# Kernel optimization log

Measured on AMD Instinct MI355X. Metric: run time of the kernel, lower is better.

The kernel has to match this reference:

```python
import jax, jax.numpy as jnp
import numpy as np
import itertools

DIMS = (128, 128, 128)
CHANNELS = 8
BATCH = 2_097_152


def setup_inputs() -> dict:
    key = jax.random.key(0)
    k1, k2 = jax.random.split(key)
    unList = jax.random.uniform(k1, (BATCH, len(DIMS)), dtype=jnp.float32)
    table = jax.random.uniform(k2, DIMS + (CHANNELS,), dtype=jnp.float32)  # initScale=1, initMode='R'
    return {"unList": unList, "table": table}


def reference(unList, table):
    # N-D multilinear (bilinear/trilinear) interpolated table lookup.
    dims = table.shape[:-1]
    n = len(dims)
    c = table.shape[-1]
    dims_f = jnp.asarray(dims, jnp.float32)
    # map normalized coords [0,1] onto grid [0, dim-1]
    scaled = jnp.clip(unList, 0.0, 1.0) * (dims_f - 1.0)          # [B, n]
    i0 = jnp.clip(jnp.floor(scaled), 0.0, dims_f - 2.0).astype(jnp.int32)  # lower corner
    frac = scaled - i0.astype(jnp.float32)                        # [B, n] in [0,1]
    # flatten grid for single-axis gathers
    strides = jnp.asarray([int(np.prod(dims[k + 1:])) for k in range(n)], jnp.int32)
    table_flat = table.reshape(-1, c)                             # [prod(dims), C]
    out = jnp.zeros((unList.shape[0], c), table.dtype)
    # loop over the 2^n corners (8 for 3D) -- small static loop
    for corner in itertools.product((0, 1), repeat=n):
        bits = jnp.asarray(corner, jnp.int32)                     # [n]
        flat_idx = ((i0 + bits) * strides).sum(-1)                # [B]
        w = jnp.prod(jnp.where(jnp.asarray(corner, bool), frac, 1.0 - frac), axis=-1)  # [B]
        out = out + w[:, None] * table_flat[flat_idx]             # gather + weighted sum
    return out
```

## Files before the change

### kernel.cpp

```cpp
#include <hip/hip_runtime.h>


#define DIM 128
#define CH 8
#define NBIN 4064
#define TBYTES 67108864u
#define CHUNK 8192
#define PPT 32
#define CUR_OFF 16384
#define BASE_OFF 32768
#define REC_OFF 65536

__device__ __forceinline__ int key_of(float ux, float uy) {
    float sx = fminf(fmaxf(ux, 0.0f), 1.0f) * 127.0f;
    float sy = fminf(fmaxf(uy, 0.0f), 1.0f) * 127.0f;
    int x0 = (int)fminf(floorf(sx), 126.0f);
    int y0 = (int)fminf(floorf(sy), 126.0f);
    return x0 * 32 + (y0 >> 2);
}

__global__ __launch_bounds__(256) void k_hist(const float* __restrict__ un,
                                              unsigned* __restrict__ hist, int batch) {
    __shared__ unsigned lh[NBIN];
    for (int i = threadIdx.x; i < NBIN; i += 256) lh[i] = 0;
    __syncthreads();
    int stride = gridDim.x * blockDim.x;
    for (int i = blockIdx.x * blockDim.x + threadIdx.x; i < batch; i += stride)
        atomicAdd(&lh[key_of(un[3 * i], un[3 * i + 1])], 1u);
    __syncthreads();
    for (int i = threadIdx.x; i < NBIN; i += 256)
        if (lh[i]) atomicAdd(&hist[i], lh[i]);
}

__global__ __launch_bounds__(1024) void k_scan(const unsigned* __restrict__ hist,
                                               unsigned* __restrict__ cursor,
                                               unsigned* __restrict__ base) {
    __shared__ unsigned s[1024];
    int t = threadIdx.x;
    int b0 = t * 4;
    unsigned loc[4], sum = 0;
#pragma unroll
    for (int j = 0; j < 4; ++j) {
        int k = b0 + j;
        unsigned h = (k < NBIN) ? hist[k] : 0u;
        loc[j] = sum;
        sum += h;
    }
    s[t] = sum;
    __syncthreads();
    for (int off = 1; off < 1024; off <<= 1) {
        unsigned v = (t >= off) ? s[t - off] : 0u;
        __syncthreads();
        s[t] += v;
        __syncthreads();
    }
    unsigned excl = s[t] - sum;
#pragma unroll
    for (int j = 0; j < 4; ++j) {
        int k = b0 + j;
        if (k < NBIN) { base[k] = excl + loc[j]; cursor[k] = excl + loc[j]; }
    }
    if (t == 1023) base[NBIN] = s[1023];
}

__global__ __launch_bounds__(256) void k_scatter(const float* __restrict__ un,
                                                 unsigned* __restrict__ cursor,
                                                 float4* __restrict__ rec, int batch) {
    __shared__ unsigned lh[NBIN];
    __shared__ unsigned lbase[NBIN];
    int t = threadIdx.x;
    for (int i = t; i < NBIN; i += 256) lh[i] = 0;
    __syncthreads();
    int start = blockIdx.x * CHUNK;
    unsigned kr[PPT];
#pragma unroll
    for (int j = 0; j < PPT; ++j) {
        int i = start + j * 256 + t;
        if (i < batch) {
            int k = key_of(un[3 * i], un[3 * i + 1]);
            unsigned r = atomicAdd(&lh[k], 1u);
            kr[j] = (unsigned)k | (r << 12);
        } else kr[j] = 0u;
    }
    __syncthreads();
    for (int i = t; i < NBIN; i += 256)
        lbase[i] = lh[i] ? atomicAdd(&cursor[i], lh[i]) : 0u;
    __syncthreads();
#pragma unroll
    for (int j = 0; j < PPT; ++j) {
        int i = start + j * 256 + t;
        if (i < batch) {
            unsigned k = kr[j] & 4095u, r = kr[j] >> 12;
            float ux = un[3 * i], uy = un[3 * i + 1], uz = un[3 * i + 2];
            rec[lbase[k] + r] = make_float4(ux, uy, uz, __uint_as_float((unsigned)i));
        }
    }
}

__global__ __launch_bounds__(256) void k_main(const float4* __restrict__ rec,
                                              const float* __restrict__ table,
                                              const unsigned* __restrict__ base,
                                              float* __restrict__ out) {
    __shared__ float4 lds4[2560];
    char* ldsb = (char*)lds4;
    const char* tb = (const char*)table;

    int g = blockIdx.x;
    int gx = g >> 5, gy2 = g & 31;
    int ybase = gy2 * 4;
    unsigned s = base[g], e = base[g + 1];

    unsigned offA = (unsigned)(gx * 128 + ybase) * 4096u;
    unsigned offB = offA + 524288u;

    for (int i = threadIdx.x; i < 1280; i += 256) {
        unsigned go = offA + (unsigned)i * 16u;
        if (go > TBYTES - 16u) go = TBYTES - 16u;
        lds4[i] = *(const float4*)(tb + go);
    }
    for (int i = threadIdx.x; i < 1280; i += 256) {
        unsigned go = offB + (unsigned)i * 16u;
        if (go > TBYTES - 16u) go = TBYTES - 16u;
        lds4[1280 + i] = *(const float4*)(tb + go);
    }
    __syncthreads();

    int t = (int)threadIdx.x;
    int lane = t & 63, wave = t >> 6;
    int p = lane >> 2, q = lane & 3;
    const float dmax = 127.0f, imax = 126.0f;
    const unsigned qoff = (unsigned)(q << 4);

    for (unsigned i0 = s + (unsigned)(wave * 16); i0 < e; i0 += 64u) {
        unsigned i = i0 + (unsigned)p;
        if (i < e) {
            float4 r = rec[i];
            unsigned orig = __float_as_uint(r.w);

            float sx = fminf(fmaxf(r.x, 0.0f), 1.0f) * dmax;
            float sy = fminf(fmaxf(r.y, 0.0f), 1.0f) * dmax;
            float sz = fminf(fmaxf(r.z, 0.0f), 1.0f) * dmax;
            float fx0 = fminf(floorf(sx), imax);
            float fy0 = fminf(floorf(sy), imax);
            float fz0 = fminf(floorf(sz), imax);
            int y0 = (int)fy0, z0 = (int)fz0;
            float fx = sx - fx0, fy = sy - fy0, fz = sz - fz0;

            float wzq = (q & 2) ? fz : (1.0f - fz);
            float gxw = 1.0f - fx, gyw = 1.0f - fy;
            float w0 = gxw * gyw * wzq;
            float w1 = gxw * fy  * wzq;
            float w2 = fx  * gyw * wzq;
            float w3 = fx  * fy  * wzq;

            int dy = y0 - ybase;
            unsigned a = (unsigned)(dy * 4096 + z0 * 32) + qoff;

            float4 v0 = *(const float4*)(ldsb + a);
            float4 v1 = *(const float4*)(ldsb + a + 4096u);
            float4 v2 = *(const float4*)(ldsb + a + 20480u);
            float4 v3 = *(const float4*)(ldsb + a + 24576u);

            float4 acc;
            acc.x = w0 * v0.x + w1 * v1.x + w2 * v2.x + w3 * v3.x;
            acc.y = w0 * v0.y + w1 * v1.y + w2 * v2.y + w3 * v3.y;
            acc.z = w0 * v0.z + w1 * v1.z + w2 * v2.z + w3 * v3.z;
            acc.w = w0 * v0.w + w1 * v1.w + w2 * v2.w + w3 * v3.w;

            acc.x += __shfl_xor(acc.x, 2);
            acc.y += __shfl_xor(acc.y, 2);
            acc.z += __shfl_xor(acc.z, 2);
            acc.w += __shfl_xor(acc.w, 2);

            if (q < 2)
                *reinterpret_cast<float4*>(out + (size_t)orig * CH + (q << 2)) = acc;
        }
    }
}

__global__ __launch_bounds__(256) void k_naive(const float* __restrict__ un,
                                               const float* __restrict__ table,
                                               float* __restrict__ out, int batch) {
    int b = blockIdx.x * blockDim.x + threadIdx.x;
    if (b >= batch) return;
    float ux = un[3 * b], uy = un[3 * b + 1], uz = un[3 * b + 2];
    const float dmax = 127.0f, imax = 126.0f;
    float sx = fminf(fmaxf(ux, 0.0f), 1.0f) * dmax;
    float sy = fminf(fmaxf(uy, 0.0f), 1.0f) * dmax;
    float sz = fminf(fmaxf(uz, 0.0f), 1.0f) * dmax;
    float fx0 = fminf(floorf(sx), imax);
    float fy0 = fminf(floorf(sy), imax);
    float fz0 = fminf(floorf(sz), imax);
    int x0 = (int)fx0, y0 = (int)fy0, z0 = (int)fz0;
    float fx = sx - fx0, fy = sy - fy0, fz = sz - fz0;
    float wx[2] = {1.0f - fx, fx};
    float wy[2] = {1.0f - fy, fy};
    float wz0 = 1.0f - fz, wz1 = fz;
    float acc[CH];
#pragma unroll
    for (int c = 0; c < CH; ++c) acc[c] = 0.0f;
#pragma unroll
    for (int bx = 0; bx < 2; ++bx)
#pragma unroll
        for (int by = 0; by < 2; ++by) {
            const float* pp = table + ((size_t)((x0 + bx) * DIM + (y0 + by)) * DIM + z0) * CH;
            float wxy = wx[bx] * wy[by];
            float w0 = wxy * wz0, w1 = wxy * wz1;
            float4 a0 = *reinterpret_cast<const float4*>(pp + 0);
            float4 a1 = *reinterpret_cast<const float4*>(pp + 4);
            float4 b0 = *reinterpret_cast<const float4*>(pp + 8);
            float4 b1 = *reinterpret_cast<const float4*>(pp + 12);
            acc[0] += w0 * a0.x + w1 * b0.x;  acc[1] += w0 * a0.y + w1 * b0.y;
            acc[2] += w0 * a0.z + w1 * b0.z;  acc[3] += w0 * a0.w + w1 * b0.w;
            acc[4] += w0 * a1.x + w1 * b1.x;  acc[5] += w0 * a1.y + w1 * b1.y;
            acc[6] += w0 * a1.z + w1 * b1.z;  acc[7] += w0 * a1.w + w1 * b1.w;
        }
    float4* o = reinterpret_cast<float4*>(out + (size_t)b * CH);
    o[0] = make_float4(acc[0], acc[1], acc[2], acc[3]);
    o[1] = make_float4(acc[4], acc[5], acc[6], acc[7]);
}

extern "C" void kernel_launch(void* const* d_in, const int* in_sizes, int n_in,
                              void* d_out, int out_size, void* d_ws, size_t ws_size,
                              hipStream_t stream) {
    const float* un    = (const float*)d_in[0];
    const float* table = (const float*)d_in[1];
    float* out         = (float*)d_out;
    int batch = in_sizes[0] / 3;

    size_t need = (size_t)REC_OFF + (size_t)batch * 16;
    if (ws_size < need) {
        int grid = (batch + 255) / 256;
        k_naive<<<grid, 256, 0, stream>>>(un, table, out, batch);
        return;
    }

    unsigned* hist   = (unsigned*)d_ws;
    unsigned* cursor = (unsigned*)((char*)d_ws + CUR_OFF);
    unsigned* base   = (unsigned*)((char*)d_ws + BASE_OFF);
    float4*   rec    = (float4*)((char*)d_ws + REC_OFF);

    hipMemsetAsync(d_ws, 0, CUR_OFF, stream);
    k_hist<<<512, 256, 0, stream>>>(un, hist, batch);
    k_scan<<<1, 1024, 0, stream>>>(hist, cursor, base);
    int nscat = (batch + CHUNK - 1) / CHUNK;
    k_scatter<<<nscat, 256, 0, stream>>>(un, cursor, rec, batch);
    k_main<<<NBIN, 256, 0, stream>>>(rec, table, base, out);
}
```

Baseline: 129.3 us.

## Swizzle LDS tile layout and software-pipeline record loads in main kernel

The table slab is now stored in LDS under an XOR swizzle of the address bits, meant to cut bank conflicts on the per-point corner reads. The two staging loops are merged into one, and blocks with no records exit right after staging. The record loop is unrolled four ways with the next four records prefetched while the current ones are processed, so global load latency overlaps with compute. The cost is more registers and possibly lower occupancy, and the prefetch clamps to the last valid index, adding redundant reads near the end of each range.

```diff
diff --git a/kernel.cpp b/kernel.cpp
--- a/kernel.cpp
+++ b/kernel.cpp
@@ -114,68 +114,82 @@
     unsigned offB = offA + 524288u;
 
     for (int i = threadIdx.x; i < 1280; i += 256) {
-        unsigned go = offA + (unsigned)i * 16u;
+        unsigned wa = (unsigned)i * 16u;
+        unsigned sa = wa ^ ((wa >> 2) & 0x60u);
+        unsigned go = offA + wa;
         if (go > TBYTES - 16u) go = TBYTES - 16u;
-        lds4[i] = *(const float4*)(tb + go);
-    }
-    for (int i = threadIdx.x; i < 1280; i += 256) {
-        unsigned go = offB + (unsigned)i * 16u;
+        *(float4*)(ldsb + sa) = *(const float4*)(tb + go);
+        go = offB + wa;
         if (go > TBYTES - 16u) go = TBYTES - 16u;
-        lds4[1280 + i] = *(const float4*)(tb + go);
-    }
-    __syncthreads();
+        *(float4*)(ldsb + 20480u + sa) = *(const float4*)(tb + go);
+    }
+    __syncthreads();
+    if (e <= s) return;
 
     int t = (int)threadIdx.x;
     int lane = t & 63, wave = t >> 6;
     int p = lane >> 2, q = lane & 3;
     const float dmax = 127.0f, imax = 126.0f;
     const unsigned qoff = (unsigned)(q << 4);
-
-    for (unsigned i0 = s + (unsigned)(wave * 16); i0 < e; i0 += 64u) {
-        unsigned i = i0 + (unsigned)p;
-        if (i < e) {
-            float4 r = rec[i];
-            unsigned orig = __float_as_uint(r.w);
-
-            float sx = fminf(fmaxf(r.x, 0.0f), 1.0f) * dmax;
-            float sy = fminf(fmaxf(r.y, 0.0f), 1.0f) * dmax;
-            float sz = fminf(fmaxf(r.z, 0.0f), 1.0f) * dmax;
-            float fx0 = fminf(floorf(sx), imax);
-            float fy0 = fminf(floorf(sy), imax);
-            float fz0 = fminf(floorf(sz), imax);
-            int y0 = (int)fy0, z0 = (int)fz0;
-            float fx = sx - fx0, fy = sy - fy0, fz = sz - fz0;
-
-            float wzq = (q & 2) ? fz : (1.0f - fz);
-            float gxw = 1.0f - fx, gyw = 1.0f - fy;
-            float w0 = gxw * gyw * wzq;
-            float w1 = gxw * fy  * wzq;
-            float w2 = fx  * gyw * wzq;
-            float w3 = fx  * fy  * wzq;
-
-            int dy = y0 - ybase;
-            unsigned a = (unsigned)(dy * 4096 + z0 * 32) + qoff;
-
-            float4 v0 = *(const float4*)(ldsb + a);
-            float4 v1 = *(const float4*)(ldsb + a + 4096u);
-            float4 v2 = *(const float4*)(ldsb + a + 20480u);
-            float4 v3 = *(const float4*)(ldsb + a + 24576u);
-
-            float4 acc;
-            acc.x = w0 * v0.x + w1 * v1.x + w2 * v2.x + w3 * v3.x;
-            acc.y = w0 * v0.y + w1 * v1.y + w2 * v2.y + w3 * v3.y;
-            acc.z = w0 * v0.z + w1 * v1.z + w2 * v2.z + w3 * v3.z;
-            acc.w = w0 * v0.w + w1 * v1.w + w2 * v2.w + w3 * v3.w;
-
-            acc.x += __shfl_xor(acc.x, 2);
-            acc.y += __shfl_xor(acc.y, 2);
-            acc.z += __shfl_xor(acc.z, 2);
-            acc.w += __shfl_xor(acc.w, 2);
-
-            if (q < 2)
-                *reinterpret_cast<float4*>(out + (size_t)orig * CH + (q << 2)) = acc;
-        }
-    }
+    const unsigned last = e - 1u;
+
+    unsigned myi = s + (unsigned)(wave * 16 + p);
+    unsigned cnt = e - s;
+
+#define PROC(rr, idx) { \
+        if ((idx) < e) { \
+            unsigned orig = __float_as_uint(rr.w); \
+            float sx = fminf(fmaxf(rr.x, 0.0f), 1.0f) * dmax; \
+            float sy = fminf(fmaxf(rr.y, 0.0f), 1.0f) * dmax; \
+            float sz = fminf(fmaxf(rr.z, 0.0f), 1.0f) * dmax; \
+            float fx0 = fminf(floorf(sx), imax); \
+            float fy0 = fminf(floorf(sy), imax); \
+            float fz0 = fminf(floorf(sz), imax); \
+            int y0 = (int)fy0, z0 = (int)fz0; \
+            float fx = sx - fx0, fy = sy - fy0, fz = sz - fz0; \
+            float wzq = (q & 2) ? fz : (1.0f - fz); \
+            float gxw = 1.0f - fx, gyw = 1.0f - fy; \
+            float w0 = gxw * gyw * wzq; \
+            float w1 = gxw * fy  * wzq; \
+            float w2 = fx  * gyw * wzq; \
+            float w3 = fx  * fy  * wzq; \
+            int dy = y0 - ybase; \
+            unsigned a = (unsigned)(dy * 4096 + z0 * 32) + qoff; \
+            unsigned sa = a ^ ((a >> 2) & 0x60u); \
+            float4 v0 = *(const float4*)(ldsb + sa); \
+            float4 v1 = *(const float4*)(ldsb + sa + 4096u); \
+            float4 v2 = *(const float4*)(ldsb + sa + 20480u); \
+            float4 v3 = *(const float4*)(ldsb + sa + 24576u); \
+            float4 acc; \
+            acc.x = w0 * v0.x + w1 * v1.x + w2 * v2.x + w3 * v3.x; \
+            acc.y = w0 * v0.y + w1 * v1.y + w2 * v2.y + w3 * v3.y; \
+            acc.z = w0 * v0.z + w1 * v1.z + w2 * v2.z + w3 * v3.z; \
+            acc.w = w0 * v0.w + w1 * v1.w + w2 * v2.w + w3 * v3.w; \
+            acc.x += __shfl_xor(acc.x, 2); \
+            acc.y += __shfl_xor(acc.y, 2); \
+            acc.z += __shfl_xor(acc.z, 2); \
+            acc.w += __shfl_xor(acc.w, 2); \
+            if (q < 2) \
+                *reinterpret_cast<float4*>(out + (size_t)orig * CH + (q << 2)) = acc; \
+        } }
+
+    float4 r0 = rec[min(myi +   0u, last)];
+    float4 r1 = rec[min(myi +  64u, last)];
+    float4 r2 = rec[min(myi + 128u, last)];
+    float4 r3 = rec[min(myi + 192u, last)];
+
+    for (unsigned c0 = 0; c0 < cnt; c0 += 256u) {
+        float4 n0 = rec[min(myi + c0 + 256u, last)];
+        float4 n1 = rec[min(myi + c0 + 320u, last)];
+        float4 n2 = rec[min(myi + c0 + 384u, last)];
+        float4 n3 = rec[min(myi + c0 + 448u, last)];
+        PROC(r0, myi + c0 +   0u)
+        PROC(r1, myi + c0 +  64u)
+        PROC(r2, myi + c0 + 128u)
+        PROC(r3, myi + c0 + 192u)
+        r0 = n0; r1 = n1; r2 = n2; r3 = n3;
+    }
+#undef PROC
 }
 
 __global__ __launch_bounds__(256) void k_naive(const float* __restrict__ un,
```

New measurement: 120.9 us. 1.07x faster.
